# Optimization experiments

Hardware: AMD Instinct MI355X
Metric: run time of the kernel (lower is better)

Reference implementation:

```python
import jax, jax.numpy as jnp
import numpy as np


def gcn_conv(x, W, b, src, dst, n):
    """PyG GCNConv: linear transform, add self-loops, symmetric deg^-1/2 norm, scatter-add."""
    h = x @ W                                   # [N, F_out]
    loop = jnp.arange(n)
    s = jnp.concatenate([src, loop])            # sources incl. self-loops
    d = jnp.concatenate([dst, loop])            # destinations incl. self-loops
    deg = jax.ops.segment_sum(jnp.ones_like(d, dtype=h.dtype), d, num_segments=n)
    inv_sqrt = jnp.where(deg > 0, jax.lax.rsqrt(deg), 0.0)
    norm = inv_sqrt[s] * inv_sqrt[d]            # [E+N]
    msgs = h[s] * norm[:, None]                 # gather + scale
    out = jax.ops.segment_sum(msgs, d, num_segments=n)  # scatter-add
    return out + b


def setup_inputs() -> dict:
    key = jax.random.key(0)
    ks = jax.random.split(key, 8)
    N, E = 100000, 1600000
    C_IN, C_HID, C_OUT = 256, 128, 64
    x = jax.random.normal(ks[0], (N, C_IN), dtype=jnp.float32)
    edge_index = jax.random.randint(ks[1], (2, E), 0, N, dtype=jnp.int64)
    W1 = jax.random.normal(ks[2], (C_IN, C_HID), dtype=jnp.float32) / np.sqrt(C_IN)
    b1 = jnp.zeros((C_HID,), dtype=jnp.float32)
    Wmu = jax.random.normal(ks[3], (C_HID, C_OUT), dtype=jnp.float32) / np.sqrt(C_HID)
    bmu = jnp.zeros((C_OUT,), dtype=jnp.float32)
    Wls = jax.random.normal(ks[4], (C_HID, C_OUT), dtype=jnp.float32) / np.sqrt(C_HID)
    bls = jnp.zeros((C_OUT,), dtype=jnp.float32)
    return {"x": x, "edge_index": edge_index, "W1": W1, "b1": b1,
            "Wmu": Wmu, "bmu": bmu, "Wls": Wls, "bls": bls}


def reference(x, edge_index, W1, b1, Wmu, bmu, Wls, bls):
    n = x.shape[0]
    src, dst = edge_index[0], edge_index[1]
    h = jax.nn.relu(gcn_conv(x, W1, b1, src, dst, n))
    mu = gcn_conv(h, Wmu, bmu, src, dst, n)
    logstd = gcn_conv(h, Wls, bls, src, dst, n)
    return mu, logstd
```

## Files before the change

### kernel.cpp

```cpp
#include <hip/hip_runtime.h>
#include <hip/hip_fp16.h>


__device__ __forceinline__ unsigned int pack_h2(float a, float b) {
    __half2 h = __floats2half2_rn(a, b);
    return *reinterpret_cast<unsigned int*>(&h);
}
__device__ __forceinline__ float2 unpack_h2(unsigned int u) {
    __half2 h = *reinterpret_cast<__half2*>(&u);
    return __half22float2(h);
}


__global__ __launch_bounds__(256) void k_hist(const int* __restrict__ dst, int E,
                                              int* __restrict__ degcnt) {
    int i = blockIdx.x * 256 + threadIdx.x;
    if (i < E) atomicAdd(&degcnt[dst[i]], 1);
}

__global__ __launch_bounds__(256) void k_deg_finalize(const int* __restrict__ degcnt,
                                                      float* __restrict__ invsqrt,
                                                      int* __restrict__ blocksums, int N) {
    __shared__ int sd[256];
    int t = threadIdx.x;
    int i = blockIdx.x * 256 + t;
    int v = (i < N) ? degcnt[i] : 0;
    if (i < N) invsqrt[i] = rsqrtf((float)(v + 1));
    sd[t] = v;
    __syncthreads();
#pragma unroll
    for (int s = 128; s > 0; s >>= 1) {
        if (t < s) sd[t] += sd[t + s];
        __syncthreads();
    }
    if (t == 0) blocksums[blockIdx.x] = sd[0];
}

__global__ __launch_bounds__(1024) void k_scan_blocks(int* blocksums, int NB) {
    __shared__ int s[1024];
    int t = threadIdx.x;
    int v = (t < NB) ? blocksums[t] : 0;
    s[t] = v;
    __syncthreads();
    for (int off = 1; off < 1024; off <<= 1) {
        int x = (t >= off) ? s[t - off] : 0;
        __syncthreads();
        s[t] += x;
        __syncthreads();
    }
    if (t < NB) blocksums[t] = s[t] - v;
}

__global__ __launch_bounds__(256) void k_rowstart(const int* __restrict__ degcnt,
                                                  const int* __restrict__ blocksums,
                                                  int* __restrict__ rowstart,
                                                  int* __restrict__ rowwork, int N, int E) {
    __shared__ int s[256];
    int t = threadIdx.x;
    int i = blockIdx.x * 256 + t;
    int v = (i < N) ? degcnt[i] : 0;
    s[t] = v;
    __syncthreads();
    for (int off = 1; off < 256; off <<= 1) {
        int x = (t >= off) ? s[t - off] : 0;
        __syncthreads();
        s[t] += x;
        __syncthreads();
    }
    if (i < N) {
        int e = s[t] - v + blocksums[blockIdx.x];
        rowstart[i] = e;
        rowwork[i] = e;
    }
    if (blockIdx.x == 0 && t == 0) rowstart[N] = E;
}

__global__ __launch_bounds__(256) void k_fill(const int* __restrict__ src,
                                              const int* __restrict__ dst, int E,
                                              const float* __restrict__ invsqrt,
                                              int* __restrict__ rowwork,
                                              uint2* __restrict__ csr_sw) {
    int i = blockIdx.x * 256 + threadIdx.x;
    if (i < E) {
        int s = src[i], d = dst[i];
        int pos = atomicAdd(&rowwork[d], 1);
        csr_sw[pos] = make_uint2((unsigned int)s, __float_as_uint(invsqrt[s]));
    }
}


#define XS_S 44
#define WS_S 140
__device__ __forceinline__ int ws_phys4(int cq) { return cq * 4 + (cq >> 3) * 4; }
__device__ __forceinline__ int ws_o(int cg) { return cg * 8 + (cg >> 2) * 4; }


__global__ __launch_bounds__(256, 4) void k_gemm1(const float* __restrict__ x,
                                                  const float* __restrict__ W,
                                                  unsigned int* __restrict__ H1, int N) {
    __shared__ __align__(16) float xs[64][XS_S];
    __shared__ __align__(16) float ws[32][WS_S];
    int t = threadIdx.x;
    int rg = t >> 4;
    int cg = t & 15;
    int row0 = blockIdx.x * 64;
    int o4 = ws_o(cg);
    float acc[4][8];
#pragma unroll
    for (int a = 0; a < 4; a++)
#pragma unroll
        for (int b = 0; b < 8; b++) acc[a][b] = 0.f;

    for (int k0 = 0; k0 < 256; k0 += 32) {
#pragma unroll
        for (int l = 0; l < 2; l++) {
            int idx = t + 256 * l;
            int rr = idx >> 3, kq = idx & 7;
            int grow = row0 + rr;
            float4 v = make_float4(0.f, 0.f, 0.f, 0.f);
            if (grow < N) v = *(const float4*)(x + (size_t)grow * 256 + k0 + kq * 4);
            *(float4*)&xs[rr][kq * 4] = v;
        }
#pragma unroll
        for (int l = 0; l < 4; l++) {
            int idx = t + 256 * l;
            int kr = idx >> 5, cq = idx & 31;
            *(float4*)&ws[kr][ws_phys4(cq)] = *(const float4*)(W + (size_t)(k0 + kr) * 128 + cq * 4);
        }
        __syncthreads();
#pragma unroll
        for (int kk = 0; kk < 32; kk++) {
            float4 wb0 = *(float4*)&ws[kk][o4];
            float4 wb1 = *(float4*)&ws[kk][o4 + 4];
            float wb[8] = {wb0.x, wb0.y, wb0.z, wb0.w, wb1.x, wb1.y, wb1.z, wb1.w};
            float xa[4];
#pragma unroll
            for (int i = 0; i < 4; i++) xa[i] = xs[rg * 4 + i][kk];
#pragma unroll
            for (int i = 0; i < 4; i++)
#pragma unroll
                for (int j = 0; j < 8; j++) acc[i][j] = fmaf(xa[i], wb[j], acc[i][j]);
        }
        __syncthreads();
    }
#pragma unroll
    for (int i = 0; i < 4; i++) {
        int grow = row0 + rg * 4 + i;
        if (grow < N) {
            uint4 st;
            st.x = pack_h2(acc[i][0], acc[i][1]);
            st.y = pack_h2(acc[i][2], acc[i][3]);
            st.z = pack_h2(acc[i][4], acc[i][5]);
            st.w = pack_h2(acc[i][6], acc[i][7]);
            *(uint4*)(H1 + (size_t)grow * 64 + cg * 4) = st;
        }
    }
}


__global__ __launch_bounds__(256, 4) void k_gemm2(const float* __restrict__ G,
                                                  const float* __restrict__ Wmu,
                                                  const float* __restrict__ bmu,
                                                  const float* __restrict__ Wls,
                                                  const float* __restrict__ bls,
                                                  float* __restrict__ omu,
                                                  float* __restrict__ ols, int N) {
    __shared__ __align__(16) float xs[64][XS_S];
    __shared__ __align__(16) float ws[32][WS_S];
    int t = threadIdx.x;
    int rg = t >> 4;
    int cg = t & 15;
    int row0 = blockIdx.x * 64;
    int o4 = ws_o(cg);
    float acc[4][8];
#pragma unroll
    for (int a = 0; a < 4; a++)
#pragma unroll
        for (int b = 0; b < 8; b++) acc[a][b] = 0.f;

    for (int k0 = 0; k0 < 128; k0 += 32) {
#pragma unroll
        for (int l = 0; l < 2; l++) {
            int idx = t + 256 * l;
            int rr = idx >> 3, kq = idx & 7;
            int grow = row0 + rr;
            float4 v = make_float4(0.f, 0.f, 0.f, 0.f);
            if (grow < N) v = *(const float4*)(G + (size_t)grow * 128 + k0 + kq * 4);
            *(float4*)&xs[rr][kq * 4] = v;
        }
#pragma unroll
        for (int l = 0; l < 4; l++) {
            int idx = t + 256 * l;
            int kr = idx >> 5, cq = idx & 31;
            const float* wp = (cq < 16) ? (Wmu + (size_t)(k0 + kr) * 64 + cq * 4)
                                        : (Wls + (size_t)(k0 + kr) * 64 + (cq - 16) * 4);
            *(float4*)&ws[kr][ws_phys4(cq)] = *(const float4*)wp;
        }
        __syncthreads();
#pragma unroll
        for (int kk = 0; kk < 32; kk++) {
            float4 wb0 = *(float4*)&ws[kk][o4];
            float4 wb1 = *(float4*)&ws[kk][o4 + 4];
            float wb[8] = {wb0.x, wb0.y, wb0.z, wb0.w, wb1.x, wb1.y, wb1.z, wb1.w};
            float xa[4];
#pragma unroll
            for (int i = 0; i < 4; i++) xa[i] = xs[rg * 4 + i][kk];
#pragma unroll
            for (int i = 0; i < 4; i++)
#pragma unroll
                for (int j = 0; j < 8; j++) acc[i][j] = fmaf(xa[i], wb[j], acc[i][j]);
        }
        __syncthreads();
    }
    int is_mu = (cg < 8);
    int ccol = (is_mu ? cg : cg - 8) * 8;
    const float* bp = is_mu ? (bmu + ccol) : (bls + ccol);
    float* ob = is_mu ? omu : ols;
    float4 b0 = *(const float4*)bp;
    float4 b1 = *(const float4*)(bp + 4);
#pragma unroll
    for (int i = 0; i < 4; i++) {
        int grow = row0 + rg * 4 + i;
        if (grow < N) {
            float4 v0 = make_float4(acc[i][0] + b0.x, acc[i][1] + b0.y,
                                    acc[i][2] + b0.z, acc[i][3] + b0.w);
            float4 v1 = make_float4(acc[i][4] + b1.x, acc[i][5] + b1.y,
                                    acc[i][6] + b1.z, acc[i][7] + b1.w);
            *(float4*)(ob + (size_t)grow * 64 + ccol) = v0;
            *(float4*)(ob + (size_t)grow * 64 + ccol + 4) = v1;
        }
    }
}


template <int MODE>
__global__ __launch_bounds__(256, 8) void k_agg(const unsigned int* __restrict__ tbl,
                                                const float* __restrict__ invsqrt,
                                                const int* __restrict__ rowstart,
                                                const uint2* __restrict__ csr,
                                                const float* __restrict__ bias,
                                                unsigned int* __restrict__ out16,
                                                float2* __restrict__ out32, int N) {
    int node = blockIdx.x * 4 + (threadIdx.x >> 6);
    int t = threadIdx.x & 63;
    if (node >= N) return;
    int start = rowstart[node], end = rowstart[node + 1];
    float isq = invsqrt[node];
    float2 v = unpack_h2(tbl[(size_t)node * 64 + t]);
    float aL = isq * v.x, aH = isq * v.y;
    for (int base = start; base < end; base += 64) {
        int cnt = end - base;
        if (cnt > 64) cnt = 64;
        uint2 e = make_uint2(0u, 0u);
        if (t < cnt) e = csr[base + t];
        int j = 0;
        for (; j + 2 <= cnt; j += 2) {
            int s0 = __shfl((int)e.x, j);
            float w0 = __int_as_float(__shfl((int)e.y, j));
            int s1 = __shfl((int)e.x, j + 1);
            float w1 = __int_as_float(__shfl((int)e.y, j + 1));
            float2 f0 = unpack_h2(tbl[(size_t)s0 * 64 + t]);
            float2 f1 = unpack_h2(tbl[(size_t)s1 * 64 + t]);
            aL = fmaf(w0, f0.x, aL);
            aH = fmaf(w0, f0.y, aH);
            aL = fmaf(w1, f1.x, aL);
            aH = fmaf(w1, f1.y, aH);
        }
        if (j < cnt) {
            int s0 = __shfl((int)e.x, j);
            float w0 = __int_as_float(__shfl((int)e.y, j));
            float2 f0 = unpack_h2(tbl[(size_t)s0 * 64 + t]);
            aL = fmaf(w0, f0.x, aL);
            aH = fmaf(w0, f0.y, aH);
        }
    }
    aL *= isq;
    aH *= isq;
    if (MODE == 1) {
        float2 b = ((const float2*)bias)[t];
        aL = fmaxf(aL + b.x, 0.f);
        aH = fmaxf(aH + b.y, 0.f);
        out16[(size_t)node * 64 + t] = pack_h2(aL, aH);
    } else {
        out32[(size_t)node * 64 + t] = make_float2(aL, aH);
    }
}


extern "C" void kernel_launch(void* const* d_in, const int* in_sizes, int n_in,
                              void* d_out, int out_size, void* d_ws, size_t ws_size,
                              hipStream_t stream) {
    const float* x   = (const float*)d_in[0];
    const int*   ei  = (const int*)d_in[1];
    const float* W1  = (const float*)d_in[2];
    const float* b1  = (const float*)d_in[3];
    const float* Wmu = (const float*)d_in[4];
    const float* bmu = (const float*)d_in[5];
    const float* Wls = (const float*)d_in[6];
    const float* bls = (const float*)d_in[7];

    int N = in_sizes[0] / 256;
    int E = in_sizes[1] / 2;
    const int* src = ei;
    const int* dst = ei + E;
    float* omu = (float*)d_out;
    float* ols = omu + (size_t)N * 64;

    char* w = (char*)d_ws;
    size_t off = 0;
    auto alloc = [&](size_t bytes) -> char* {
        char* p = w + off;
        off = (off + bytes + 255) & ~(size_t)255;
        return p;
    };
    int*          degcnt    = (int*)alloc((size_t)N * 4);
    float*        invsqrt   = (float*)alloc((size_t)N * 4);
    int*          rowstart  = (int*)alloc((size_t)(N + 1) * 4);
    int*          rowwork   = (int*)alloc((size_t)N * 4);
    int*          blocksums = (int*)alloc(4096);
    uint2*        csr_sw    = (uint2*)alloc((size_t)E * 8);
    unsigned int* H1f16     = (unsigned int*)alloc((size_t)N * 64 * 4);
    unsigned int* Hf16      = (unsigned int*)alloc((size_t)N * 64 * 4);
    float*        G2        = (float*)alloc((size_t)N * 128 * 4);

    int NB = (N + 255) / 256;

    hipMemsetAsync(degcnt, 0, (size_t)N * 4, stream);
    k_hist<<<(E + 255) / 256, 256, 0, stream>>>(dst, E, degcnt);
    k_deg_finalize<<<NB, 256, 0, stream>>>(degcnt, invsqrt, blocksums, N);
    k_scan_blocks<<<1, 1024, 0, stream>>>(blocksums, NB);
    k_rowstart<<<NB, 256, 0, stream>>>(degcnt, blocksums, rowstart, rowwork, N, E);
    k_fill<<<(E + 255) / 256, 256, 0, stream>>>(src, dst, E, invsqrt, rowwork, csr_sw);

    k_gemm1<<<(N + 63) / 64, 256, 0, stream>>>(x, W1, H1f16, N);
    k_agg<1><<<(N + 3) / 4, 256, 0, stream>>>(H1f16, invsqrt, rowstart, csr_sw, b1,
                                              Hf16, nullptr, N);
    k_agg<0><<<(N + 3) / 4, 256, 0, stream>>>(Hf16, invsqrt, rowstart, csr_sw, nullptr,
                                              nullptr, (float2*)G2, N);
    k_gemm2<<<(N + 63) / 64, 256, 0, stream>>>(G2, Wmu, bmu, Wls, bls, omu, ols, N);
}
```

Measured before the change: 574.6 us.

## Replace FP32 SIMT GEMMs with split-bf16 MFMA GEMMs

```diff
diff --git a/kernel.cpp b/kernel.cpp
--- a/kernel.cpp
+++ b/kernel.cpp
@@ -1,5 +1,8 @@
 #include <hip/hip_runtime.h>
 #include <hip/hip_fp16.h>
+
+typedef short bf16x8 __attribute__((ext_vector_type(8)));
+typedef float f32x4 __attribute__((ext_vector_type(4)));
 
 
 __device__ __forceinline__ unsigned int pack_h2(float a, float b) {
@@ -9,6 +12,18 @@
 __device__ __forceinline__ float2 unpack_h2(unsigned int u) {
     __half2 h = *reinterpret_cast<__half2*>(&u);
     return __half22float2(h);
+}
+__device__ __forceinline__ unsigned short f2bf(float f) {
+    unsigned int u = __float_as_uint(f);
+    unsigned int r = (u + 0x7FFFu + ((u >> 16) & 1u)) >> 16;
+    return (unsigned short)r;
+}
+__device__ __forceinline__ float bf2f(unsigned short h) {
+    return __uint_as_float((unsigned int)h << 16);
+}
+__device__ __forceinline__ unsigned short f2h_bits(float f) {
+    __half h = __float2half_rn(f);
+    return *reinterpret_cast<unsigned short*>(&h);
 }
 
 
@@ -89,145 +104,134 @@
 }
 
 
-#define XS_S 44
-#define WS_S 140
-__device__ __forceinline__ int ws_phys4(int cq) { return cq * 4 + (cq >> 3) * 4; }
-__device__ __forceinline__ int ws_o(int cg) { return cg * 8 + (cg >> 2) * 4; }
-
-
-__global__ __launch_bounds__(256, 4) void k_gemm1(const float* __restrict__ x,
-                                                  const float* __restrict__ W,
-                                                  unsigned int* __restrict__ H1, int N) {
-    __shared__ __align__(16) float xs[64][XS_S];
-    __shared__ __align__(16) float ws[32][WS_S];
+__global__ __launch_bounds__(256) void k_wprep(const float* __restrict__ W1,
+                                               const float* __restrict__ Wmu,
+                                               const float* __restrict__ Wls,
+                                               unsigned short* __restrict__ w1t_hi,
+                                               unsigned short* __restrict__ w1t_lo,
+                                               unsigned short* __restrict__ w2t_hi,
+                                               unsigned short* __restrict__ w2t_lo) {
+    int i = blockIdx.x * 256 + threadIdx.x;
+    if (i < 256 * 128) {
+        int k = i >> 7, c = i & 127;
+        float w = W1[k * 128 + c];
+        unsigned short hi = f2bf(w);
+        unsigned short lo = f2bf(w - bf2f(hi));
+        w1t_hi[c * 256 + k] = hi;
+        w1t_lo[c * 256 + k] = lo;
+    } else {
+        int j = i - 256 * 128;
+        if (j < 128 * 128) {
+            int k = j >> 7, c = j & 127;
+            float w = (c < 64) ? Wmu[k * 64 + c] : Wls[k * 64 + (c - 64)];
+            unsigned short hi = f2bf(w);
+            unsigned short lo = f2bf(w - bf2f(hi));
+            w2t_hi[c * 128 + k] = hi;
+            w2t_lo[c * 128 + k] = lo;
+        }
+    }
+}
+
+
+template <int KTOT, int MODE>
+__global__ __launch_bounds__(256) void k_gemm_mfma(const float* __restrict__ A,
+                                                   const unsigned short* __restrict__ Bh,
+                                                   const unsigned short* __restrict__ Bl,
+                                                   const float* __restrict__ bmu,
+                                                   const float* __restrict__ bls,
+                                                   unsigned short* __restrict__ o16,
+                                                   float* __restrict__ omu,
+                                                   float* __restrict__ ols, int N) {
+    __shared__ __align__(16) unsigned short As_hi[128 * 40];
+    __shared__ __align__(16) unsigned short As_lo[128 * 40];
+    __shared__ __align__(16) unsigned short Bs_hi[128 * 40];
+    __shared__ __align__(16) unsigned short Bs_lo[128 * 40];
+
     int t = threadIdx.x;
-    int rg = t >> 4;
-    int cg = t & 15;
-    int row0 = blockIdx.x * 64;
-    int o4 = ws_o(cg);
-    float acc[4][8];
+    int l = t & 63;
+    int w = t >> 6;
+    int wm = (w >> 1) * 64;
+    int wn = (w & 1) * 64;
+    int lr = l & 15;
+    int lc = l >> 4;
+    int row0 = blockIdx.x * 128;
+
+    f32x4 acc[4][4];
 #pragma unroll
     for (int a = 0; a < 4; a++)
 #pragma unroll
-        for (int b = 0; b < 8; b++) acc[a][b] = 0.f;
-
-    for (int k0 = 0; k0 < 256; k0 += 32) {
-#pragma unroll
-        for (int l = 0; l < 2; l++) {
-            int idx = t + 256 * l;
+        for (int b = 0; b < 4; b++) acc[a][b] = (f32x4){0.f, 0.f, 0.f, 0.f};
+
+    for (int k0 = 0; k0 < KTOT; k0 += 32) {
+#pragma unroll
+        for (int it = 0; it < 4; it++) {
+            int idx = t + 256 * it;
             int rr = idx >> 3, kq = idx & 7;
             int grow = row0 + rr;
             float4 v = make_float4(0.f, 0.f, 0.f, 0.f);
-            if (grow < N) v = *(const float4*)(x + (size_t)grow * 256 + k0 + kq * 4);
-            *(float4*)&xs[rr][kq * 4] = v;
-        }
-#pragma unroll
-        for (int l = 0; l < 4; l++) {
-            int idx = t + 256 * l;
-            int kr = idx >> 5, cq = idx & 31;
-            *(float4*)&ws[kr][ws_phys4(cq)] = *(const float4*)(W + (size_t)(k0 + kr) * 128 + cq * 4);
-        }
-        __syncthreads();
-#pragma unroll
-        for (int kk = 0; kk < 32; kk++) {
-            float4 wb0 = *(float4*)&ws[kk][o4];
-            float4 wb1 = *(float4*)&ws[kk][o4 + 4];
-            float wb[8] = {wb0.x, wb0.y, wb0.z, wb0.w, wb1.x, wb1.y, wb1.z, wb1.w};
-            float xa[4];
-#pragma unroll
-            for (int i = 0; i < 4; i++) xa[i] = xs[rg * 4 + i][kk];
-#pragma unroll
-            for (int i = 0; i < 4; i++)
-#pragma unroll
-                for (int j = 0; j < 8; j++) acc[i][j] = fmaf(xa[i], wb[j], acc[i][j]);
-        }
-        __syncthreads();
-    }
-#pragma unroll
-    for (int i = 0; i < 4; i++) {
-        int grow = row0 + rg * 4 + i;
-        if (grow < N) {
-            uint4 st;
-            st.x = pack_h2(acc[i][0], acc[i][1]);
-            st.y = pack_h2(acc[i][2], acc[i][3]);
-            st.z = pack_h2(acc[i][4], acc[i][5]);
-            st.w = pack_h2(acc[i][6], acc[i][7]);
-            *(uint4*)(H1 + (size_t)grow * 64 + cg * 4) = st;
-        }
-    }
-}
-
-
-__global__ __launch_bounds__(256, 4) void k_gemm2(const float* __restrict__ G,
-                                                  const float* __restrict__ Wmu,
-                                                  const float* __restrict__ bmu,
-                                                  const float* __restrict__ Wls,
-                                                  const float* __restrict__ bls,
-                                                  float* __restrict__ omu,
-                                                  float* __restrict__ ols, int N) {
-    __shared__ __align__(16) float xs[64][XS_S];
-    __shared__ __align__(16) float ws[32][WS_S];
-    int t = threadIdx.x;
-    int rg = t >> 4;
-    int cg = t & 15;
-    int row0 = blockIdx.x * 64;
-    int o4 = ws_o(cg);
-    float acc[4][8];
-#pragma unroll
-    for (int a = 0; a < 4; a++)
-#pragma unroll
-        for (int b = 0; b < 8; b++) acc[a][b] = 0.f;
-
-    for (int k0 = 0; k0 < 128; k0 += 32) {
-#pragma unroll
-        for (int l = 0; l < 2; l++) {
-            int idx = t + 256 * l;
-            int rr = idx >> 3, kq = idx & 7;
-            int grow = row0 + rr;
-            float4 v = make_float4(0.f, 0.f, 0.f, 0.f);
-            if (grow < N) v = *(const float4*)(G + (size_t)grow * 128 + k0 + kq * 4);
-            *(float4*)&xs[rr][kq * 4] = v;
-        }
-#pragma unroll
-        for (int l = 0; l < 4; l++) {
-            int idx = t + 256 * l;
-            int kr = idx >> 5, cq = idx & 31;
-            const float* wp = (cq < 16) ? (Wmu + (size_t)(k0 + kr) * 64 + cq * 4)
-                                        : (Wls + (size_t)(k0 + kr) * 64 + (cq - 16) * 4);
-            *(float4*)&ws[kr][ws_phys4(cq)] = *(const float4*)wp;
-        }
-        __syncthreads();
-#pragma unroll
-        for (int kk = 0; kk < 32; kk++) {
-            float4 wb0 = *(float4*)&ws[kk][o4];
-            float4 wb1 = *(float4*)&ws[kk][o4 + 4];
-            float wb[8] = {wb0.x, wb0.y, wb0.z, wb0.w, wb1.x, wb1.y, wb1.z, wb1.w};
-            float xa[4];
-#pragma unroll
-            for (int i = 0; i < 4; i++) xa[i] = xs[rg * 4 + i][kk];
-#pragma unroll
-            for (int i = 0; i < 4; i++)
-#pragma unroll
-                for (int j = 0; j < 8; j++) acc[i][j] = fmaf(xa[i], wb[j], acc[i][j]);
-        }
-        __syncthreads();
-    }
-    int is_mu = (cg < 8);
-    int ccol = (is_mu ? cg : cg - 8) * 8;
-    const float* bp = is_mu ? (bmu + ccol) : (bls + ccol);
-    float* ob = is_mu ? omu : ols;
-    float4 b0 = *(const float4*)bp;
-    float4 b1 = *(const float4*)(bp + 4);
-#pragma unroll
-    for (int i = 0; i < 4; i++) {
-        int grow = row0 + rg * 4 + i;
-        if (grow < N) {
-            float4 v0 = make_float4(acc[i][0] + b0.x, acc[i][1] + b0.y,
-                                    acc[i][2] + b0.z, acc[i][3] + b0.w);
-            float4 v1 = make_float4(acc[i][4] + b1.x, acc[i][5] + b1.y,
-                                    acc[i][6] + b1.z, acc[i][7] + b1.w);
-            *(float4*)(ob + (size_t)grow * 64 + ccol) = v0;
-            *(float4*)(ob + (size_t)grow * 64 + ccol + 4) = v1;
+            if (grow < N) v = *(const float4*)(A + (size_t)grow * KTOT + k0 + kq * 4);
+            ushort4 h, lo;
+            h.x = f2bf(v.x); lo.x = f2bf(v.x - bf2f(h.x));
+            h.y = f2bf(v.y); lo.y = f2bf(v.y - bf2f(h.y));
+            h.z = f2bf(v.z); lo.z = f2bf(v.z - bf2f(h.z));
+            h.w = f2bf(v.w); lo.w = f2bf(v.w - bf2f(h.w));
+            *(ushort4*)&As_hi[rr * 40 + kq * 4] = h;
+            *(ushort4*)&As_lo[rr * 40 + kq * 4] = lo;
+        }
+#pragma unroll
+        for (int it = 0; it < 2; it++) {
+            int idx = t + 256 * it;
+            int col = idx >> 2, ck = idx & 3;
+            uint4 vh = *(const uint4*)(Bh + (size_t)col * KTOT + k0 + ck * 8);
+            uint4 vl = *(const uint4*)(Bl + (size_t)col * KTOT + k0 + ck * 8);
+            *(uint4*)&Bs_hi[col * 40 + ck * 8] = vh;
+            *(uint4*)&Bs_lo[col * 40 + ck * 8] = vl;
+        }
+        __syncthreads();
+
+        bf16x8 ah[4], al[4];
+#pragma unroll
+        for (int mf = 0; mf < 4; mf++) {
+            int r = wm + mf * 16 + lr;
+            ah[mf] = *(bf16x8*)&As_hi[r * 40 + lc * 8];
+            al[mf] = *(bf16x8*)&As_lo[r * 40 + lc * 8];
+        }
+#pragma unroll
+        for (int nf = 0; nf < 4; nf++) {
+            int c = wn + nf * 16 + lr;
+            bf16x8 bh = *(bf16x8*)&Bs_hi[c * 40 + lc * 8];
+            bf16x8 bl = *(bf16x8*)&Bs_lo[c * 40 + lc * 8];
+#pragma unroll
+            for (int mf = 0; mf < 4; mf++)
+                acc[mf][nf] = __builtin_amdgcn_mfma_f32_16x16x32_bf16(ah[mf], bh, acc[mf][nf], 0, 0, 0);
+#pragma unroll
+            for (int mf = 0; mf < 4; mf++)
+                acc[mf][nf] = __builtin_amdgcn_mfma_f32_16x16x32_bf16(ah[mf], bl, acc[mf][nf], 0, 0, 0);
+#pragma unroll
+            for (int mf = 0; mf < 4; mf++)
+                acc[mf][nf] = __builtin_amdgcn_mfma_f32_16x16x32_bf16(al[mf], bh, acc[mf][nf], 0, 0, 0);
+        }
+        __syncthreads();
+    }
+
+#pragma unroll
+    for (int mf = 0; mf < 4; mf++) {
+#pragma unroll
+        for (int nf = 0; nf < 4; nf++) {
+            int col = wn + nf * 16 + lr;
+#pragma unroll
+            for (int r = 0; r < 4; r++) {
+                int row = row0 + wm + mf * 16 + lc * 4 + r;
+                if (row < N) {
+                    float v = acc[mf][nf][r];
+                    if (MODE == 1) {
+                        o16[(size_t)row * 128 + col] = f2h_bits(v);
+                    } else {
+                        if (col < 64) omu[(size_t)row * 64 + col] = v + bmu[col];
+                        else          ols[(size_t)row * 64 + (col - 64)] = v + bls[col - 64];
+                    }
+                }
+            }
         }
     }
 }
@@ -313,29 +317,37 @@
         off = (off + bytes + 255) & ~(size_t)255;
         return p;
     };
-    int*          degcnt    = (int*)alloc((size_t)N * 4);
-    float*        invsqrt   = (float*)alloc((size_t)N * 4);
-    int*          rowstart  = (int*)alloc((size_t)(N + 1) * 4);
-    int*          rowwork   = (int*)alloc((size_t)N * 4);
-    int*          blocksums = (int*)alloc(4096);
-    uint2*        csr_sw    = (uint2*)alloc((size_t)E * 8);
-    unsigned int* H1f16     = (unsigned int*)alloc((size_t)N * 64 * 4);
-    unsigned int* Hf16      = (unsigned int*)alloc((size_t)N * 64 * 4);
-    float*        G2        = (float*)alloc((size_t)N * 128 * 4);
+    int*            degcnt    = (int*)alloc((size_t)N * 4);
+    float*          invsqrt   = (float*)alloc((size_t)N * 4);
+    int*            rowstart  = (int*)alloc((size_t)(N + 1) * 4);
+    int*            rowwork   = (int*)alloc((size_t)N * 4);
+    int*            blocksums = (int*)alloc(4096);
+    uint2*          csr_sw    = (uint2*)alloc((size_t)E * 8);
+    unsigned int*   H1f16     = (unsigned int*)alloc((size_t)N * 64 * 4);
+    unsigned int*   Hf16      = (unsigned int*)alloc((size_t)N * 64 * 4);
+    float*          G2        = (float*)alloc((size_t)N * 128 * 4);
+    unsigned short* w1t_hi    = (unsigned short*)alloc(128 * 256 * 2);
+    unsigned short* w1t_lo    = (unsigned short*)alloc(128 * 256 * 2);
+    unsigned short* w2t_hi    = (unsigned short*)alloc(128 * 128 * 2);
+    unsigned short* w2t_lo    = (unsigned short*)alloc(128 * 128 * 2);
 
     int NB = (N + 255) / 256;
 
     hipMemsetAsync(degcnt, 0, (size_t)N * 4, stream);
+    k_wprep<<<192, 256, 0, stream>>>(W1, Wmu, Wls, w1t_hi, w1t_lo, w2t_hi, w2t_lo);
     k_hist<<<(E + 255) / 256, 256, 0, stream>>>(dst, E, degcnt);
     k_deg_finalize<<<NB, 256, 0, stream>>>(degcnt, invsqrt, blocksums, N);
     k_scan_blocks<<<1, 1024, 0, stream>>>(blocksums, NB);
     k_rowstart<<<NB, 256, 0, stream>>>(degcnt, blocksums, rowstart, rowwork, N, E);
     k_fill<<<(E + 255) / 256, 256, 0, stream>>>(src, dst, E, invsqrt, rowwork, csr_sw);
 
-    k_gemm1<<<(N + 63) / 64, 256, 0, stream>>>(x, W1, H1f16, N);
+    int GB = (N + 127) / 128;
+    k_gemm_mfma<256, 1><<<GB, 256, 0, stream>>>(x, w1t_hi, w1t_lo, nullptr, nullptr,
+                                                (unsigned short*)H1f16, nullptr, nullptr, N);
     k_agg<1><<<(N + 3) / 4, 256, 0, stream>>>(H1f16, invsqrt, rowstart, csr_sw, b1,
                                               Hf16, nullptr, N);
     k_agg<0><<<(N + 3) / 4, 256, 0, stream>>>(Hf16, invsqrt, rowstart, csr_sw, nullptr,
                                               nullptr, (float2*)G2, N);
-    k_gemm2<<<(N + 63) / 64, 256, 0, stream>>>(G2, Wmu, bmu, Wls, bls, omu, ols, N);
-}
+    k_gemm_mfma<128, 2><<<GB, 256, 0, stream>>>(G2, w2t_hi, w2t_lo, bmu, bls,
+                                                nullptr, omu, ols, N);
+}
```

Measured after the change: 557.9 us. 1.03x faster.
